# Kernel tuning notes

Measured on AMD Instinct MI355X. Metric: run time of the kernel, lower is better.

Reference implementation:

```python
import jax, jax.numpy as jnp
import numpy as np

SIM_THRESHOLD = 0.5   # similarity_threshold
LAMBDA = 0.1          # lambda_weight default


def setup_inputs() -> dict:
    key = jax.random.key(0)
    ks = jax.random.split(key, 8)
    B, T, C, P = 8, 1024, 1024, 100
    return {
        "attention_scores": jax.random.normal(ks[0], (B, T, T), jnp.float32),
        "context": jax.random.normal(ks[1], (B, C), jnp.float32),
        "triggers": jax.random.normal(ks[2], (P, C), jnp.float32),
        "biases": jax.random.uniform(ks[3], (P, T, T), jnp.float32),
        "confidences": jnp.ones((P,), jnp.float32),
        "W1": jax.random.normal(ks[4], (2 * C, C), jnp.float32) * (1.0 / np.sqrt(2 * C)),
        "b1": jnp.zeros((C,), jnp.float32),
        "W2": jax.random.normal(ks[5], (C,), jnp.float32) * (1.0 / np.sqrt(C)),
        "b2": jnp.zeros((1,), jnp.float32),
    }


def reference(attention_scores, context, triggers, biases, confidences, W1, b1, W2, b2):
    C = context.shape[-1]
    # combined = cat([context, trigger]) @ W1 == context @ W1[:C] + trigger @ W1[C:]
    ctx_h = context @ W1[:C]              # (B, C)
    trg_h = triggers @ W1[C:]             # (P, C)
    h = jax.nn.relu(ctx_h[:, None, :] + trg_h[None, :, :] + b1)   # (B, P, C)
    logits = h @ W2 + b2[0]               # (B, P)
    scores = jax.nn.sigmoid(logits).mean(axis=0)                  # (P,) mean over batch
    # match: only patterns with score > threshold contribute, weighted by score*confidence
    weights = jnp.where(scores > SIM_THRESHOLD, scores * confidences, 0.0)  # (P,)
    reasoning_bias = jnp.einsum("p,pij->ij", weights, biases)     # (T, T)
    return attention_scores + LAMBDA * reasoning_bias[None, :, :]
```

## Files before the change

### kernel.cpp

```cpp
#include <hip/hip_runtime.h>
#include <hip/hip_bf16.h>
#include <math.h>

#define BD 8
#define TD 1024
#define CD 1024
#define PD 100
#define KS 16
#define KW (CD / KS)
#define LAMBDA 0.1f
#define SIM_THR 0.5f

typedef float f4 __attribute__((ext_vector_type(4)));

__device__ float g_pctx[KS][BD][CD];
__device__ float g_ptrg[KS][PD][CD];
__device__ float g_wd[PD];

__global__ __launch_bounds__(256) void hidden_kernel(const float* __restrict__ context,
                                                     const float* __restrict__ triggers,
                                                     const float* __restrict__ W1) {
    const int c  = blockIdx.x * 256 + threadIdx.x;
    const int kz = blockIdx.z;
    const int k0 = kz * KW;
    const bool is_ctx = (blockIdx.y == 0);
    const int  ych = blockIdx.y - 1;
    const float* __restrict__ W1p = is_ctx ? W1 : (W1 + (size_t)CD * CD);
    const float* __restrict__ src = is_ctx ? context : (triggers + (size_t)ych * 10 * CD);
    float* __restrict__ dst = is_ctx ? &g_pctx[kz][0][0] : &g_ptrg[kz][ych * 10][0];
    const int nrows = is_ctx ? 8 : 10;

    __shared__ float s_src[10][KW];
    for (int t = threadIdx.x; t < 10 * KW; t += 256) {
        const int r = t >> 6, k = t & (KW - 1);
        s_src[r][k] = src[(size_t)(r < nrows ? r : 0) * CD + k0 + k];
    }
    __syncthreads();

    float acc[10];
#pragma unroll
    for (int i = 0; i < 10; ++i) acc[i] = 0.f;

#pragma unroll 8
    for (int kk = 0; kk < KW; ++kk) {
        const float wv = W1p[(size_t)(k0 + kk) * CD + c];
#pragma unroll
        for (int i = 0; i < 10; ++i)
            acc[i] = fmaf(s_src[i][kk], wv, acc[i]);
    }
#pragma unroll
    for (int i = 0; i < 10; ++i)
        if (i < nrows) dst[(size_t)i * CD + c] = acc[i];
}

__global__ __launch_bounds__(512) void score_kernel(const float* __restrict__ b1,
                                                    const float* __restrict__ W2,
                                                    const float* __restrict__ b2,
                                                    const float* __restrict__ conf) {
    const int p = blockIdx.x;
    __shared__ float s_h[CD];
    __shared__ float s_logit[BD];

    for (int c = threadIdx.x; c < CD; c += 512) {
        float v = b1[c];
#pragma unroll
        for (int kz = 0; kz < KS; ++kz) v += g_ptrg[kz][p][c];
        s_h[c] = v;
    }
    __syncthreads();

    const int b = threadIdx.x >> 6, lane = threadIdx.x & 63;
    float sum = 0.f;
    for (int c = lane; c < CD; c += 64) {
        float v = s_h[c];
#pragma unroll
        for (int kz = 0; kz < KS; ++kz) v += g_pctx[kz][b][c];
        sum = fmaf(fmaxf(v, 0.f), W2[c], sum);
    }
#pragma unroll
    for (int off = 32; off > 0; off >>= 1) sum += __shfl_down(sum, off);
    if (lane == 0) s_logit[b] = sum + b2[0];
    __syncthreads();
    if (threadIdx.x == 0) {
        float s = 0.f;
#pragma unroll
        for (int bb = 0; bb < BD; ++bb) s += 1.f / (1.f + expf(-s_logit[bb]));
        s *= (1.f / BD);
        g_wd[p] = (s > SIM_THR) ? s * conf[p] * LAMBDA : 0.f;
    }
}

__global__ __launch_bounds__(256) void out_kernel(const float* __restrict__ attn,
                                                  const float* __restrict__ biases,
                                                  float* __restrict__ out) {
    __shared__ float s_w[PD];
    __shared__ unsigned long long s_off[PD];
    __shared__ int s_n;
    if (threadIdx.x < PD) s_w[threadIdx.x] = g_wd[threadIdx.x];
    __syncthreads();
    if (threadIdx.x == 0) {
        int n = 0;
        for (int q = 0; q < PD; ++q)
            if (s_w[q] != 0.f) {
                s_w[n] = s_w[q];
                s_off[n] = (unsigned long long)q * (TD * TD);
                ++n;
            }
        s_n = n;
    }
    __syncthreads();
    const int n = s_n;

    const size_t rowoff = (size_t)blockIdx.x * TD + (size_t)threadIdx.x * 4;

    f4 av[BD];
#pragma unroll
    for (int b = 0; b < BD; ++b)
        av[b] = *(const f4*)(attn + (size_t)b * TD * TD + rowoff);

    f4 acc = {0.f, 0.f, 0.f, 0.f};
    int t = 0;
    for (; t + 8 <= n; t += 8) {
        float w[8];
        const f4* p[8];
#pragma unroll
        for (int u = 0; u < 8; ++u) {
            w[u] = s_w[t + u];
            p[u] = (const f4*)(biases + (size_t)s_off[t + u] + rowoff);
        }
        f4 v[8];
#pragma unroll
        for (int u = 0; u < 8; ++u) v[u] = *p[u];
#pragma unroll
        for (int u = 0; u < 8; ++u) {
            acc.x = fmaf(w[u], v[u].x, acc.x);
            acc.y = fmaf(w[u], v[u].y, acc.y);
            acc.z = fmaf(w[u], v[u].z, acc.z);
            acc.w = fmaf(w[u], v[u].w, acc.w);
        }
    }
    for (; t < n; ++t) {
        const float w = s_w[t];
        const f4 bv = *(const f4*)(biases + (size_t)s_off[t] + rowoff);
        acc.x = fmaf(w, bv.x, acc.x);
        acc.y = fmaf(w, bv.y, acc.y);
        acc.z = fmaf(w, bv.z, acc.z);
        acc.w = fmaf(w, bv.w, acc.w);
    }

#pragma unroll
    for (int b = 0; b < BD; ++b) {
        f4 ov = av[b] + acc;
        __builtin_nontemporal_store(ov, (f4*)(out + (size_t)b * TD * TD + rowoff));
    }
}

extern "C" void kernel_launch(void* const* d_in, const int* in_sizes, int n_in,
                              void* d_out, int out_size, void* d_ws, size_t ws_size,
                              hipStream_t stream) {
    const float* attn     = (const float*)d_in[0];
    const float* context  = (const float*)d_in[1];
    const float* triggers = (const float*)d_in[2];
    const float* biases   = (const float*)d_in[3];
    const float* conf     = (const float*)d_in[4];
    const float* W1       = (const float*)d_in[5];
    const float* b1       = (const float*)d_in[6];
    const float* W2       = (const float*)d_in[7];
    const float* b2       = (const float*)d_in[8];
    float* out = (float*)d_out;

    hipLaunchKernelGGL(hidden_kernel, dim3(CD / 256, 11, KS), dim3(256), 0, stream,
                       context, triggers, W1);
    hipLaunchKernelGGL(score_kernel, dim3(PD), dim3(512), 0, stream, b1, W2, b2, conf);
    hipLaunchKernelGGL(out_kernel, dim3(TD), dim3(256), 0, stream, attn, biases, out);
}
```

Baseline: 108.8 us.

## Hoist pattern compaction into separate kernel and use finer-grained output blocks

Moves the serial compaction of nonzero pattern weights out of every out_kernel block into a one-thread compact_kernel, so each block only loads a precompacted list. The output kernel now handles 2 floats per thread with 2048 blocks, uses 32-bit offsets, and unrolls by 4 with a launch-bounds occupancy hint. The goal is to remove per-block serial work and raise occupancy and memory-level parallelism, at the cost of one extra launch and narrower loads.

```diff
diff --git a/kernel.cpp b/kernel.cpp
--- a/kernel.cpp
+++ b/kernel.cpp
@@ -11,11 +11,15 @@
 #define LAMBDA 0.1f
 #define SIM_THR 0.5f
 
+typedef float f2 __attribute__((ext_vector_type(2)));
 typedef float f4 __attribute__((ext_vector_type(4)));
 
-__device__ float g_pctx[KS][BD][CD];
-__device__ float g_ptrg[KS][PD][CD];
-__device__ float g_wd[PD];
+__device__ float    g_pctx[KS][BD][CD];
+__device__ float    g_ptrg[KS][PD][CD];
+__device__ float    g_wd[PD];
+__device__ float    g_wc[PD];
+__device__ unsigned g_poff[PD];
+__device__ int      g_nnz;
 
 __global__ __launch_bounds__(256) void hidden_kernel(const float* __restrict__ context,
                                                      const float* __restrict__ triggers,
@@ -90,68 +94,62 @@
     }
 }
 
-__global__ __launch_bounds__(256) void out_kernel(const float* __restrict__ attn,
-                                                  const float* __restrict__ biases,
-                                                  float* __restrict__ out) {
-    __shared__ float s_w[PD];
-    __shared__ unsigned long long s_off[PD];
-    __shared__ int s_n;
-    if (threadIdx.x < PD) s_w[threadIdx.x] = g_wd[threadIdx.x];
-    __syncthreads();
+__global__ void compact_kernel() {
     if (threadIdx.x == 0) {
         int n = 0;
-        for (int q = 0; q < PD; ++q)
-            if (s_w[q] != 0.f) {
-                s_w[n] = s_w[q];
-                s_off[n] = (unsigned long long)q * (TD * TD);
+        for (int q = 0; q < PD; ++q) {
+            const float w = g_wd[q];
+            if (w != 0.f) {
+                g_wc[n]   = w;
+                g_poff[n] = (unsigned)(q * (TD * TD));
                 ++n;
             }
-        s_n = n;
+        }
+        g_nnz = n;
+    }
+}
+
+__global__ __launch_bounds__(256, 8) void out_kernel(const float* __restrict__ attn,
+                                                     const float* __restrict__ biases,
+                                                     float* __restrict__ out) {
+    __shared__ float    s_w[PD];
+    __shared__ unsigned s_off[PD];
+    const int n = g_nnz;
+    if (threadIdx.x < n) {
+        s_w[threadIdx.x]   = g_wc[threadIdx.x];
+        s_off[threadIdx.x] = g_poff[threadIdx.x];
     }
     __syncthreads();
-    const int n = s_n;
 
-    const size_t rowoff = (size_t)blockIdx.x * TD + (size_t)threadIdx.x * 4;
+    const size_t base = (size_t)blockIdx.x * 512 + (size_t)threadIdx.x * 2;
 
-    f4 av[BD];
+    f2 av[BD];
 #pragma unroll
     for (int b = 0; b < BD; ++b)
-        av[b] = *(const f4*)(attn + (size_t)b * TD * TD + rowoff);
+        av[b] = *(const f2*)(attn + (size_t)b * TD * TD + base);
 
-    f4 acc = {0.f, 0.f, 0.f, 0.f};
+    f2 acc = {0.f, 0.f};
     int t = 0;
-    for (; t + 8 <= n; t += 8) {
-        float w[8];
-        const f4* p[8];
-#pragma unroll
-        for (int u = 0; u < 8; ++u) {
-            w[u] = s_w[t + u];
-            p[u] = (const f4*)(biases + (size_t)s_off[t + u] + rowoff);
-        }
-        f4 v[8];
-#pragma unroll
-        for (int u = 0; u < 8; ++u) v[u] = *p[u];
-#pragma unroll
-        for (int u = 0; u < 8; ++u) {
-            acc.x = fmaf(w[u], v[u].x, acc.x);
-            acc.y = fmaf(w[u], v[u].y, acc.y);
-            acc.z = fmaf(w[u], v[u].z, acc.z);
-            acc.w = fmaf(w[u], v[u].w, acc.w);
-        }
+    for (; t + 4 <= n; t += 4) {
+        const float w0 = s_w[t + 0], w1 = s_w[t + 1], w2 = s_w[t + 2], w3 = s_w[t + 3];
+        const f2 v0 = *(const f2*)(biases + (size_t)s_off[t + 0] + base);
+        const f2 v1 = *(const f2*)(biases + (size_t)s_off[t + 1] + base);
+        const f2 v2 = *(const f2*)(biases + (size_t)s_off[t + 2] + base);
+        const f2 v3 = *(const f2*)(biases + (size_t)s_off[t + 3] + base);
+        acc.x = fmaf(w0, v0.x, fmaf(w1, v1.x, fmaf(w2, v2.x, fmaf(w3, v3.x, acc.x))));
+        acc.y = fmaf(w0, v0.y, fmaf(w1, v1.y, fmaf(w2, v2.y, fmaf(w3, v3.y, acc.y))));
     }
     for (; t < n; ++t) {
         const float w = s_w[t];
-        const f4 bv = *(const f4*)(biases + (size_t)s_off[t] + rowoff);
+        const f2 bv = *(const f2*)(biases + (size_t)s_off[t] + base);
         acc.x = fmaf(w, bv.x, acc.x);
         acc.y = fmaf(w, bv.y, acc.y);
-        acc.z = fmaf(w, bv.z, acc.z);
-        acc.w = fmaf(w, bv.w, acc.w);
     }
 
 #pragma unroll
     for (int b = 0; b < BD; ++b) {
-        f4 ov = av[b] + acc;
-        __builtin_nontemporal_store(ov, (f4*)(out + (size_t)b * TD * TD + rowoff));
+        f2 ov = av[b] + acc;
+        __builtin_nontemporal_store(ov, (f2*)(out + (size_t)b * TD * TD + base));
     }
 }
 
@@ -172,5 +170,6 @@
     hipLaunchKernelGGL(hidden_kernel, dim3(CD / 256, 11, KS), dim3(256), 0, stream,
                        context, triggers, W1);
     hipLaunchKernelGGL(score_kernel, dim3(PD), dim3(512), 0, stream, b1, W2, b2, conf);
-    hipLaunchKernelGGL(out_kernel, dim3(TD), dim3(256), 0, stream, attn, biases, out);
+    hipLaunchKernelGGL(compact_kernel, dim3(1), dim3(64), 0, stream);
+    hipLaunchKernelGGL(out_kernel, dim3(2048), dim3(256), 0, stream, attn, biases, out);
 }
```

Result: no change. 109.5 us (+0.7%).
